# Kernel optimization log

Hardware: AMD Instinct MI355X
Metric: run time of the kernel (lower is better)

Reference implementation:

```python
import jax, jax.numpy as jnp
import numpy as np

B, N, C, H = 32, 197, 768, 12
D = C // H  # head dim = 64


def setup_inputs() -> dict:
    key = jax.random.key(0)
    ks = jax.random.split(key, 5)
    std = 0.02
    x = jax.random.normal(ks[0], (B, N, C), dtype=jnp.float32)
    w_qkv = jax.random.normal(ks[1], (C, 3 * C), dtype=jnp.float32) * std
    w_proj = jax.random.normal(ks[2], (C, C), dtype=jnp.float32) * std
    b_proj = jnp.zeros((C,), dtype=jnp.float32)
    # 1x1 convs over the head axis of the attention map (Conv2d(H,H,1,bias=False))
    w_conv_l = jax.random.normal(ks[3], (H, H), dtype=jnp.float32) * std + jnp.eye(H, dtype=jnp.float32)
    w_conv_w = jax.random.normal(ks[4], (H, H), dtype=jnp.float32) * std + jnp.eye(H, dtype=jnp.float32)
    return {"x": x, "w_qkv": w_qkv, "w_proj": w_proj, "b_proj": b_proj,
            "w_conv_l": w_conv_l, "w_conv_w": w_conv_w}


def reference(x, w_qkv, w_proj, b_proj, w_conv_l, w_conv_w):
    b, n, c = x.shape
    h, d = H, c // H
    scale = d ** (-0.5)
    qkv = (x @ w_qkv).reshape(b, n, 3, h, d).transpose(2, 0, 3, 1, 4)  # [3,B,H,N,D]
    q, k, v = qkv[0], qkv[1], qkv[2]
    # value_map branch (control_output.need_value_map=True)
    value_map = jax.nn.softmax(jnp.einsum('bhnd,bhmd->bhnm', v, v) * scale, axis=-1)
    # scaled QK^T
    attn = jnp.einsum('bhnd,bhmd->bhnm', q * scale, k)  # [B,H,N,N]
    attention_scores = attn  # need_attn_score=True (captured pre-conv)
    # conv_l: 1x1 conv mixing heads
    attn = jnp.einsum('oh,bhnm->bonm', w_conv_l, attn)
    attention_probs = jax.nn.softmax(attn, axis=-1)  # need_attn_prob=True
    # conv_w: 1x1 conv mixing heads on the probabilities
    attn_w = jnp.einsum('oh,bhnm->bonm', w_conv_w, attention_probs)
    out = jnp.einsum('bhnm,bhmd->bhnd', attn_w, v)  # [B,H,N,D]
    out = out.transpose(0, 2, 1, 3).reshape(b, n, c)
    attention_output = out @ w_proj + b_proj
    return attention_output, attention_scores, attention_probs, value_map
```

## Files before the change

kernel.cpp:

```cpp
#include <hip/hip_runtime.h>
#include <cmath>

#define B_ 32
#define N_ 197
#define C_ 768
#define H_ 12
#define D_ 64
#define M_ (B_*N_)
#define MPAD_ 6400
#define K3_ (3*C_)
#define NN_ (N_*N_)
#define BH_ (B_*H_)
#define NP_ 208
#define KP_ 224
#define SCALE 0.125f

typedef __bf16 bf16x8 __attribute__((ext_vector_type(8)));
typedef __bf16 bf16x4 __attribute__((ext_vector_type(4)));
typedef float  f32x4  __attribute__((ext_vector_type(4)));

__device__ __forceinline__ void gl_lds16(const void* g, void* l) {
    __builtin_amdgcn_global_load_lds(
        (const __attribute__((address_space(1))) void*)g,
        (__attribute__((address_space(3))) void*)l,
        16, 0, 0);
}

__global__ __launch_bounds__(256) void cast_x_kernel(const float* __restrict__ X,
        __bf16* __restrict__ Xb) {
    const long long i = ((long long)blockIdx.x * 256 + threadIdx.x) * 4;
    if (i >= (long long)MPAD_ * 768) return;
    bf16x4 o;
    if (i < (long long)M_ * 768) {
        float4 f = *(const float4*)&X[i];
        o.x = (__bf16)f.x; o.y = (__bf16)f.y; o.z = (__bf16)f.z; o.w = (__bf16)f.w;
    } else {
        o.x = o.y = o.z = o.w = (__bf16)0.f;
    }
    *(bf16x4*)&Xb[i] = o;
}

__global__ __launch_bounds__(256) void transpose_cast(const float* __restrict__ W,
        __bf16* __restrict__ Wt, int R, int Ccols) {
    __shared__ float t[32][33];
    const int c0 = blockIdx.x * 32;
    const int r0 = blockIdx.y * 32;
    const int tx = threadIdx.x & 31, ty = threadIdx.x >> 5;
    #pragma unroll
    for (int i = ty; i < 32; i += 8)
        t[i][tx] = W[(size_t)(r0 + i) * Ccols + c0 + tx];
    __syncthreads();
    #pragma unroll
    for (int i = ty; i < 32; i += 8)
        Wt[(size_t)(c0 + i) * R + r0 + tx] = (__bf16)t[tx][i];
}

__global__ __launch_bounds__(256) void mfma_qkv(const __bf16* __restrict__ Xb,
        const __bf16* __restrict__ Wt, __bf16* __restrict__ q,
        __bf16* __restrict__ k, __bf16* __restrict__ v) {
    __shared__ __bf16 As[128*32];
    __shared__ __bf16 Bs[128*32];
    const int tid = threadIdx.x;
    const int wv = tid >> 6, ln = tid & 63;
    const int R0 = blockIdx.x * 128;
    const int C0 = blockIdx.y * 128;
    const int wm = wv >> 1, wn = wv & 1;
    const int arow = ln >> 2, akg = ln & 3;
    f32x4 acc[4][4] = {};
    for (int k0 = 0; k0 < 768; k0 += 32) {
        __syncthreads();
        #pragma unroll
        for (int s = 0; s < 2; s++) {
            const int seg = wv + s*4;
            const int row = seg*16 + arow;
            gl_lds16(Xb + (size_t)(R0 + row)*768 + k0 + akg*8,
                     (char*)As + seg*1024 + ln*16);
            gl_lds16(Wt + (size_t)(C0 + row)*768 + k0 + akg*8,
                     (char*)Bs + seg*1024 + ln*16);
        }
        __syncthreads();
        bf16x8 af[4], bfr[4];
        #pragma unroll
        for (int t = 0; t < 4; t++) {
            af[t]  = *(const bf16x8*)((const char*)As +
                        (wm*64 + t*16 + (ln & 15))*64 + (ln >> 4)*16);
            bfr[t] = *(const bf16x8*)((const char*)Bs +
                        (wn*64 + t*16 + (ln & 15))*64 + (ln >> 4)*16);
        }
        #pragma unroll
        for (int i = 0; i < 4; i++)
            #pragma unroll
            for (int j = 0; j < 4; j++)
                acc[i][j] = __builtin_amdgcn_mfma_f32_16x16x32_bf16(
                                af[i], bfr[j], acc[i][j], 0, 0, 0);
    }
    const int lr = (ln >> 4) * 4;
    const int lc = ln & 15;
    #pragma unroll
    for (int j = 0; j < 4; j++) {
        const int c = C0 + wn*64 + j*16 + lc;
        const int which = c / 768;
        const int rem = c - which*768;
        const int h = rem >> 6, d = rem & 63;
        __bf16* dst = (which == 0) ? q : ((which == 1) ? k : v);
        #pragma unroll
        for (int i = 0; i < 4; i++) {
            #pragma unroll
            for (int rr = 0; rr < 4; rr++) {
                const int r = R0 + wm*64 + i*16 + lr + rr;
                if (r < M_) {
                    const int bb = r / N_, n = r - bb*N_;
                    dst[(((size_t)(bb*H_ + h))*N_ + n)*64 + d] =
                        (__bf16)acc[i][j][rr];
                }
            }
        }
    }
}

__global__ __launch_bounds__(256) void mfma_proj(const __bf16* __restrict__ Ab,
        const __bf16* __restrict__ Wt, const float* __restrict__ bias,
        float* __restrict__ Y) {
    __shared__ __bf16 As[128*32];
    __shared__ __bf16 Bs[128*32];
    const int tid = threadIdx.x;
    const int wv = tid >> 6, ln = tid & 63;
    const int R0 = blockIdx.x * 128;
    const int C0 = blockIdx.y * 128;
    const int wm = wv >> 1, wn = wv & 1;
    const int arow = ln >> 2, akg = ln & 3;
    f32x4 acc[4][4] = {};
    for (int k0 = 0; k0 < 768; k0 += 32) {
        __syncthreads();
        #pragma unroll
        for (int s = 0; s < 2; s++) {
            const int seg = wv + s*4;
            const int row = seg*16 + arow;
            gl_lds16(Ab + (size_t)(R0 + row)*768 + k0 + akg*8,
                     (char*)As + seg*1024 + ln*16);
            gl_lds16(Wt + (size_t)(C0 + row)*768 + k0 + akg*8,
                     (char*)Bs + seg*1024 + ln*16);
        }
        __syncthreads();
        bf16x8 af[4], bfr[4];
        #pragma unroll
        for (int t = 0; t < 4; t++) {
            af[t]  = *(const bf16x8*)((const char*)As +
                        (wm*64 + t*16 + (ln & 15))*64 + (ln >> 4)*16);
            bfr[t] = *(const bf16x8*)((const char*)Bs +
                        (wn*64 + t*16 + (ln & 15))*64 + (ln >> 4)*16);
        }
        #pragma unroll
        for (int i = 0; i < 4; i++)
            #pragma unroll
            for (int j = 0; j < 4; j++)
                acc[i][j] = __builtin_amdgcn_mfma_f32_16x16x32_bf16(
                                af[i], bfr[j], acc[i][j], 0, 0, 0);
    }
    const int lr = (ln >> 4) * 4;
    const int lc = ln & 15;
    #pragma unroll
    for (int j = 0; j < 4; j++) {
        const int c = C0 + wn*64 + j*16 + lc;
        const float bv = bias[c];
        #pragma unroll
        for (int i = 0; i < 4; i++) {
            #pragma unroll
            for (int rr = 0; rr < 4; rr++) {
                const int r = R0 + wm*64 + i*16 + lr + rr;
                if (r < M_) Y[(size_t)r*768 + c] = acc[i][j][rr] + bv;
            }
        }
    }
}

__global__ __launch_bounds__(256) void qkt_vvt(const __bf16* __restrict__ Q,
        const __bf16* __restrict__ Km, const __bf16* __restrict__ V,
        float* __restrict__ S, float* __restrict__ VM) {
    __shared__ __bf16 Al[NP_*64];
    __shared__ __bf16 Bl[NP_*64];
    const int tid = threadIdx.x;
    const int w = tid >> 6, L = tid & 63;
    const int lm = L & 15, lg = L >> 4;
    if (blockIdx.x < BH_) {
        const int bh = blockIdx.x;
        const __bf16* Qb = Q  + (size_t)bh*N_*D_;
        const __bf16* Kb = Km + (size_t)bh*N_*D_;
        for (int i = tid*8; i < NP_*64; i += 2048) {
            const int row = i >> 6;
            bf16x8 z = {};
            *(bf16x8*)&Al[i] = (row < N_) ? *(const bf16x8*)&Qb[i] : z;
            *(bf16x8*)&Bl[i] = (row < N_) ? *(const bf16x8*)&Kb[i] : z;
        }
        __syncthreads();
        for (int rt = w; rt < 13; rt += 4) {
            const bf16x8 a0 = *(const bf16x8*)&Al[(rt*16+lm)*64 + lg*8];
            const bf16x8 a1 = *(const bf16x8*)&Al[(rt*16+lm)*64 + 32 + lg*8];
            const int rbase = rt*16 + lg*4;
            for (int ct = 0; ct < 13; ct++) {
                const bf16x8 b0 = *(const bf16x8*)&Bl[(ct*16+lm)*64 + lg*8];
                const bf16x8 b1 = *(const bf16x8*)&Bl[(ct*16+lm)*64 + 32 + lg*8];
                f32x4 acc = {};
                acc = __builtin_amdgcn_mfma_f32_16x16x32_bf16(a0, b0, acc, 0, 0, 0);
                acc = __builtin_amdgcn_mfma_f32_16x16x32_bf16(a1, b1, acc, 0, 0, 0);
                const int c = ct*16 + lm;
                if (c < N_) {
                    #pragma unroll
                    for (int r = 0; r < 4; r++) {
                        const int row = rbase + r;
                        if (row < N_)
                            S[((size_t)bh*N_ + row)*N_ + c] = acc[r] * SCALE;
                    }
                }
            }
        }
    } else {
        const int bh = blockIdx.x - BH_;
        const __bf16* Vb = V + (size_t)bh*N_*D_;
        for (int i = tid*8; i < NP_*64; i += 2048) {
            const int row = i >> 6;
            bf16x8 z = {};
            *(bf16x8*)&Al[i] = (row < N_) ? *(const bf16x8*)&Vb[i] : z;
        }
        __syncthreads();
        for (int rt = w; rt < 13; rt += 4) {
            const bf16x8 a0 = *(const bf16x8*)&Al[(rt*16+lm)*64 + lg*8];
            const bf16x8 a1 = *(const bf16x8*)&Al[(rt*16+lm)*64 + 32 + lg*8];
            f32x4 acc[13];
            for (int ct = 0; ct < 13; ct++) {
                const bf16x8 b0 = *(const bf16x8*)&Al[(ct*16+lm)*64 + lg*8];
                const bf16x8 b1 = *(const bf16x8*)&Al[(ct*16+lm)*64 + 32 + lg*8];
                f32x4 a = {};
                a = __builtin_amdgcn_mfma_f32_16x16x32_bf16(a0, b0, a, 0, 0, 0);
                a = __builtin_amdgcn_mfma_f32_16x16x32_bf16(a1, b1, a, 0, 0, 0);
                acc[ct] = a;
            }
            float mx[4] = {-1e30f, -1e30f, -1e30f, -1e30f};
            #pragma unroll
            for (int ct = 0; ct < 13; ct++) {
                const bool valid = (ct*16 + lm) < N_;
                #pragma unroll
                for (int r = 0; r < 4; r++) {
                    float val = valid ? acc[ct][r] * SCALE : -1e30f;
                    acc[ct][r] = val;
                    mx[r] = fmaxf(mx[r], val);
                }
            }
            #pragma unroll
            for (int r = 0; r < 4; r++) {
                #pragma unroll
                for (int off = 1; off < 16; off <<= 1)
                    mx[r] = fmaxf(mx[r], __shfl_xor(mx[r], off));
            }
            float sm[4] = {0.f, 0.f, 0.f, 0.f};
            #pragma unroll
            for (int ct = 0; ct < 13; ct++)
                #pragma unroll
                for (int r = 0; r < 4; r++) {
                    const float e = __expf(acc[ct][r] - mx[r]);
                    acc[ct][r] = e;
                    sm[r] += e;
                }
            #pragma unroll
            for (int r = 0; r < 4; r++) {
                #pragma unroll
                for (int off = 1; off < 16; off <<= 1)
                    sm[r] += __shfl_xor(sm[r], off);
                sm[r] = 1.f / sm[r];
            }
            const int rbase = rt*16 + lg*4;
            for (int ct = 0; ct < 13; ct++) {
                const int c = ct*16 + lm;
                if (c < N_) {
                    #pragma unroll
                    for (int r = 0; r < 4; r++) {
                        const int row = rbase + r;
                        if (row < N_)
                            VM[((size_t)bh*N_ + row)*N_ + c] = acc[ct][r] * sm[r];
                    }
                }
            }
        }
    }
}

__global__ __launch_bounds__(256) void convl_convw(const float* __restrict__ SC,
        const float* __restrict__ wl, const float* __restrict__ ww,
        float* __restrict__ PR, __bf16* __restrict__ AW) {
    __shared__ float raw[12*200];
    __shared__ float mixed[12*200];
    __shared__ float wls[144];
    __shared__ float wws[144];
    const int tid = threadIdx.x;
    const int b = blockIdx.x / N_;
    const int n = blockIdx.x - b * N_;
    if (tid < 144) { wls[tid] = wl[tid]; wws[tid] = ww[tid]; }
    for (int i = tid; i < 12*N_; i += 256) {
        int h = i / N_, m = i - h*N_;
        raw[h*200 + m] = SC[(((size_t)(b*12 + h))*N_ + n)*N_ + m];
    }
    __syncthreads();
    for (int i = tid; i < 12*N_; i += 256) {
        int o = i / N_, m = i - o*N_;
        float s = 0.f;
        #pragma unroll
        for (int h = 0; h < 12; h++) s += wls[o*12 + h] * raw[h*200 + m];
        mixed[o*200 + m] = s;
    }
    __syncthreads();
    const int w = tid >> 6, l = tid & 63;
    for (int j = 0; j < 3; j++) {
        const int o = w*3 + j;
        float vv[4];
        float mx = -1e30f;
        #pragma unroll
        for (int c = 0; c < 4; c++) {
            int m = l + 64*c;
            vv[c] = (m < N_) ? mixed[o*200 + m] : -1e30f;
            mx = fmaxf(mx, vv[c]);
        }
        #pragma unroll
        for (int off = 32; off; off >>= 1) mx = fmaxf(mx, __shfl_xor(mx, off));
        float s = 0.f;
        #pragma unroll
        for (int c = 0; c < 4; c++) {
            int m = l + 64*c;
            if (m < N_) { vv[c] = __expf(vv[c] - mx); s += vv[c]; }
        }
        #pragma unroll
        for (int off = 32; off; off >>= 1) s += __shfl_xor(s, off);
        const float inv = 1.f / s;
        float* Prow = PR + (((size_t)(b*12 + o))*N_ + n)*N_;
        #pragma unroll
        for (int c = 0; c < 4; c++) {
            int m = l + 64*c;
            if (m < N_) {
                const float p = vv[c] * inv;
                Prow[m] = p;
                raw[o*200 + m] = p;
            }
        }
    }
    __syncthreads();
    for (int i = tid; i < 12*KP_; i += 256) {
        int o = i / KP_, m = i - o*KP_;
        float s = 0.f;
        if (m < N_) {
            #pragma unroll
            for (int h = 0; h < 12; h++) s += wws[o*12 + h] * raw[h*200 + m];
        }
        AW[((size_t)(b*12 + o)*N_ + n)*KP_ + m] = (__bf16)s;
    }
}

__global__ __launch_bounds__(256) void av_mfma(const __bf16* __restrict__ AW,
        const __bf16* __restrict__ V, __bf16* __restrict__ OP) {
    __shared__ __bf16 Vt[64*KP_];
    const int tid = threadIdx.x, bh = blockIdx.x;
    const int w = tid >> 6, L = tid & 63;
    for (int i = tid*8; i < 64*KP_; i += 2048) {
        bf16x8 z = {};
        *(bf16x8*)&Vt[i] = z;
    }
    __syncthreads();
    const __bf16* Vb = V + (size_t)bh*N_*D_;
    for (int i = tid*8; i < N_*D_; i += 2048) {
        const int row = i >> 6, col = i & 63;
        const bf16x8 vv = *(const bf16x8*)&Vb[i];
        #pragma unroll
        for (int j = 0; j < 8; j++) Vt[(col+j)*KP_ + row] = vv[j];
    }
    __syncthreads();
    const int lm = L & 15, lg = L >> 4;
    const int b = bh / H_, h = bh - b*H_;
    const __bf16* Ab = AW + (size_t)bh*N_*KP_;
    for (int rt = w; rt < 13; rt += 4) {
        int ar = rt*16 + lm;
        if (ar >= N_) ar = 0;
        f32x4 acc[4] = {};
        #pragma unroll
        for (int k0 = 0; k0 < KP_; k0 += 32) {
            const bf16x8 a = *(const bf16x8*)&Ab[(size_t)ar*KP_ + k0 + lg*8];
            #pragma unroll
            for (int ct = 0; ct < 4; ct++) {
                const bf16x8 bf = *(const bf16x8*)&Vt[(ct*16+lm)*KP_ + k0 + lg*8];
                acc[ct] = __builtin_amdgcn_mfma_f32_16x16x32_bf16(
                              a, bf, acc[ct], 0, 0, 0);
            }
        }
        const int rbase = rt*16 + lg*4;
        #pragma unroll
        for (int ct = 0; ct < 4; ct++) {
            const int d = ct*16 + lm;
            #pragma unroll
            for (int r = 0; r < 4; r++) {
                const int row = rbase + r;
                if (row < N_)
                    OP[((size_t)(b*N_ + row))*C_ + h*64 + d] = (__bf16)acc[ct][r];
            }
        }
    }
}

extern "C" void kernel_launch(void* const* d_in, const int* in_sizes, int n_in,
                              void* d_out, int out_size, void* d_ws, size_t ws_size,
                              hipStream_t stream) {
    const float* x      = (const float*)d_in[0];
    const float* w_qkv  = (const float*)d_in[1];
    const float* w_proj = (const float*)d_in[2];
    const float* b_proj = (const float*)d_in[3];
    const float* w_cl   = (const float*)d_in[4];
    const float* w_cw   = (const float*)d_in[5];

    float* out    = (float*)d_out;
    float* scores = out    + (size_t)M_ * C_;
    float* probs  = scores + (size_t)BH_ * NN_;
    float* vmap   = probs  + (size_t)BH_ * NN_;

    char* base = (char*)d_ws;
    const size_t QS = (size_t)BH_ * N_ * D_;
    __bf16* q   = (__bf16*)base;
    __bf16* k   = q + QS;
    __bf16* v   = k + QS;
    __bf16* Xb  = v + QS;
    __bf16* OPb = Xb;
    __bf16* Wqt = Xb + (size_t)MPAD_*768;
    __bf16* Wpt = Wqt + (size_t)K3_*768;
    __bf16* aw  = Wpt + (size_t)768*768;

    cast_x_kernel <<<(MPAD_*768/4 + 255)/256, 256, 0, stream>>>(x, Xb);
    transpose_cast<<<dim3(72, 24),  256, 0, stream>>>(w_qkv,  Wqt, 768, K3_);
    transpose_cast<<<dim3(24, 24),  256, 0, stream>>>(w_proj, Wpt, 768, 768);

    mfma_qkv      <<<dim3(50, 18),  256, 0, stream>>>(Xb, Wqt, q, k, v);
    qkt_vvt       <<<2*BH_,         256, 0, stream>>>(q, k, v, scores, vmap);
    convl_convw   <<<M_,            256, 0, stream>>>(scores, w_cl, w_cw, probs, aw);
    av_mfma       <<<BH_,           256, 0, stream>>>(aw, v, OPb);
    mfma_proj     <<<dim3(50, 6),   256, 0, stream>>>(OPb, Wpt, b_proj, out);
}
```

Baseline: 383.2 us.

## Swizzle LDS layouts and transpose MFMA operands for vectorized score stores

Applies XOR swizzles to the LDS tiles in qkt_vvt and to the transposed V tile in av_mfma, padding the latter to a 256-element stride, to avoid LDS bank conflicts on fragment reads. The QK^T and VV^T MFMAs swap operand order so each lane holds four consecutive columns of one row. This allows 16-byte row stores of scores and value_map instead of scattered scalar stores. The value_map softmax now reduces across lanes with two shuffles instead of four, and each wave keeps its Q fragments in registers while looping over K tiles. Unaligned vector stores and the remapped indexing add correctness risk.

After: 388.9 us. About the same (+1.5%).

```diff
diff --git a/kernel.cpp b/kernel.cpp
--- a/kernel.cpp
+++ b/kernel.cpp
@@ -13,11 +13,13 @@
 #define BH_ (B_*H_)
 #define NP_ 208
 #define KP_ 224
+#define VTS_ 256
 #define SCALE 0.125f
 
 typedef __bf16 bf16x8 __attribute__((ext_vector_type(8)));
 typedef __bf16 bf16x4 __attribute__((ext_vector_type(4)));
 typedef float  f32x4  __attribute__((ext_vector_type(4)));
+typedef float  f32x4u __attribute__((ext_vector_type(4), aligned(4)));
 
 __device__ __forceinline__ void gl_lds16(const void* g, void* l) {
     __builtin_amdgcn_global_load_lds(
@@ -188,28 +190,44 @@
         const __bf16* Kb = Km + (size_t)bh*N_*D_;
         for (int i = tid*8; i < NP_*64; i += 2048) {
             const int row = i >> 6;
+            const int di = (i & ~63) | ((((i >> 3) & 7) ^ (row & 7)) << 3);
             bf16x8 z = {};
-            *(bf16x8*)&Al[i] = (row < N_) ? *(const bf16x8*)&Qb[i] : z;
-            *(bf16x8*)&Bl[i] = (row < N_) ? *(const bf16x8*)&Kb[i] : z;
-        }
-        __syncthreads();
-        for (int rt = w; rt < 13; rt += 4) {
-            const bf16x8 a0 = *(const bf16x8*)&Al[(rt*16+lm)*64 + lg*8];
-            const bf16x8 a1 = *(const bf16x8*)&Al[(rt*16+lm)*64 + 32 + lg*8];
-            const int rbase = rt*16 + lg*4;
-            for (int ct = 0; ct < 13; ct++) {
-                const bf16x8 b0 = *(const bf16x8*)&Bl[(ct*16+lm)*64 + lg*8];
-                const bf16x8 b1 = *(const bf16x8*)&Bl[(ct*16+lm)*64 + 32 + lg*8];
+            *(bf16x8*)&Al[di] = (row < N_) ? *(const bf16x8*)&Qb[i] : z;
+            *(bf16x8*)&Bl[di] = (row < N_) ? *(const bf16x8*)&Kb[i] : z;
+        }
+        __syncthreads();
+        const bool isw0 = (w == 0);
+        int nts[4];
+        nts[0] = w; nts[1] = w + 4; nts[2] = w + 8; nts[3] = isw0 ? 12 : w;
+        bf16x8 qf0[4], qf1[4];
+        #pragma unroll
+        for (int t = 0; t < 4; t++) {
+            const int qr = nts[t]*16 + lm;
+            qf0[t] = *(const bf16x8*)&Al[qr*64 + ((lg ^ (qr & 7)) << 3)];
+            qf1[t] = *(const bf16x8*)&Al[qr*64 + (((4 + lg) ^ (qr & 7)) << 3)];
+        }
+        for (int mt = 0; mt < 13; mt++) {
+            const int kr = mt*16 + lm;
+            const bf16x8 k0 = *(const bf16x8*)&Bl[kr*64 + ((lg ^ (kr & 7)) << 3)];
+            const bf16x8 k1 = *(const bf16x8*)&Bl[kr*64 + (((4 + lg) ^ (kr & 7)) << 3)];
+            const int m0 = mt*16 + lg*4;
+            #pragma unroll
+            for (int t = 0; t < 4; t++) {
                 f32x4 acc = {};
-                acc = __builtin_amdgcn_mfma_f32_16x16x32_bf16(a0, b0, acc, 0, 0, 0);
-                acc = __builtin_amdgcn_mfma_f32_16x16x32_bf16(a1, b1, acc, 0, 0, 0);
-                const int c = ct*16 + lm;
-                if (c < N_) {
-                    #pragma unroll
-                    for (int r = 0; r < 4; r++) {
-                        const int row = rbase + r;
-                        if (row < N_)
-                            S[((size_t)bh*N_ + row)*N_ + c] = acc[r] * SCALE;
+                acc = __builtin_amdgcn_mfma_f32_16x16x32_bf16(k0, qf0[t], acc, 0, 0, 0);
+                acc = __builtin_amdgcn_mfma_f32_16x16x32_bf16(k1, qf1[t], acc, 0, 0, 0);
+                const int n = nts[t]*16 + lm;
+                if ((t < 3 || isw0) && n < N_) {
+                    float* Srow = S + ((size_t)bh*N_ + n)*N_;
+                    if (m0 + 3 < N_) {
+                        f32x4 st;
+                        #pragma unroll
+                        for (int r = 0; r < 4; r++) st[r] = acc[r] * SCALE;
+                        *(f32x4u*)&Srow[m0] = st;
+                    } else {
+                        #pragma unroll
+                        for (int r = 0; r < 4; r++)
+                            if (m0 + r < N_) Srow[m0 + r] = acc[r] * SCALE;
                     }
                 }
             }
@@ -219,65 +237,65 @@
         const __bf16* Vb = V + (size_t)bh*N_*D_;
         for (int i = tid*8; i < NP_*64; i += 2048) {
             const int row = i >> 6;
+            const int di = (i & ~63) | ((((i >> 3) & 7) ^ (row & 7)) << 3);
             bf16x8 z = {};
-            *(bf16x8*)&Al[i] = (row < N_) ? *(const bf16x8*)&Vb[i] : z;
-        }
-        __syncthreads();
-        for (int rt = w; rt < 13; rt += 4) {
-            const bf16x8 a0 = *(const bf16x8*)&Al[(rt*16+lm)*64 + lg*8];
-            const bf16x8 a1 = *(const bf16x8*)&Al[(rt*16+lm)*64 + 32 + lg*8];
+            *(bf16x8*)&Al[di] = (row < N_) ? *(const bf16x8*)&Vb[i] : z;
+        }
+        __syncthreads();
+        for (int nt = w; nt < 13; nt += 4) {
+            const int qr = nt*16 + lm;
+            const bf16x8 q0 = *(const bf16x8*)&Al[qr*64 + ((lg ^ (qr & 7)) << 3)];
+            const bf16x8 q1 = *(const bf16x8*)&Al[qr*64 + (((4 + lg) ^ (qr & 7)) << 3)];
             f32x4 acc[13];
-            for (int ct = 0; ct < 13; ct++) {
-                const bf16x8 b0 = *(const bf16x8*)&Al[(ct*16+lm)*64 + lg*8];
-                const bf16x8 b1 = *(const bf16x8*)&Al[(ct*16+lm)*64 + 32 + lg*8];
+            for (int mt = 0; mt < 13; mt++) {
+                const int kr = mt*16 + lm;
+                const bf16x8 a0 = *(const bf16x8*)&Al[kr*64 + ((lg ^ (kr & 7)) << 3)];
+                const bf16x8 a1 = *(const bf16x8*)&Al[kr*64 + (((4 + lg) ^ (kr & 7)) << 3)];
                 f32x4 a = {};
-                a = __builtin_amdgcn_mfma_f32_16x16x32_bf16(a0, b0, a, 0, 0, 0);
-                a = __builtin_amdgcn_mfma_f32_16x16x32_bf16(a1, b1, a, 0, 0, 0);
-                acc[ct] = a;
-            }
-            float mx[4] = {-1e30f, -1e30f, -1e30f, -1e30f};
-            #pragma unroll
-            for (int ct = 0; ct < 13; ct++) {
-                const bool valid = (ct*16 + lm) < N_;
+                a = __builtin_amdgcn_mfma_f32_16x16x32_bf16(a0, q0, a, 0, 0, 0);
+                a = __builtin_amdgcn_mfma_f32_16x16x32_bf16(a1, q1, a, 0, 0, 0);
+                acc[mt] = a;
+            }
+            #pragma unroll
+            for (int mt = 0; mt < 13; mt++)
+                #pragma unroll
+                for (int r = 0; r < 4; r++) acc[mt][r] *= SCALE;
+            #pragma unroll
+            for (int r = 0; r < 4; r++)
+                if (192 + lg*4 + r >= N_) acc[12][r] = -1e30f;
+            float mx = -1e30f;
+            #pragma unroll
+            for (int mt = 0; mt < 13; mt++)
+                #pragma unroll
+                for (int r = 0; r < 4; r++) mx = fmaxf(mx, acc[mt][r]);
+            mx = fmaxf(mx, __shfl_xor(mx, 16));
+            mx = fmaxf(mx, __shfl_xor(mx, 32));
+            float sm = 0.f;
+            #pragma unroll
+            for (int mt = 0; mt < 13; mt++)
                 #pragma unroll
                 for (int r = 0; r < 4; r++) {
-                    float val = valid ? acc[ct][r] * SCALE : -1e30f;
-                    acc[ct][r] = val;
-                    mx[r] = fmaxf(mx[r], val);
+                    const float e = __expf(acc[mt][r] - mx);
+                    acc[mt][r] = e;
+                    sm += e;
                 }
-            }
-            #pragma unroll
-            for (int r = 0; r < 4; r++) {
+            sm += __shfl_xor(sm, 16);
+            sm += __shfl_xor(sm, 32);
+            const float inv = 1.f / sm;
+            const int n = qr;
+            if (n < N_) {
+                float* Vrow = VM + ((size_t)bh*N_ + n)*N_;
                 #pragma unroll
-                for (int off = 1; off < 16; off <<= 1)
-                    mx[r] = fmaxf(mx[r], __shfl_xor(mx[r], off));
-            }
-            float sm[4] = {0.f, 0.f, 0.f, 0.f};
-            #pragma unroll
-            for (int ct = 0; ct < 13; ct++)
+                for (int mt = 0; mt < 12; mt++) {
+                    f32x4 st;
+                    #pragma unroll
+                    for (int r = 0; r < 4; r++) st[r] = acc[mt][r] * inv;
+                    *(f32x4u*)&Vrow[mt*16 + lg*4] = st;
+                }
                 #pragma unroll
                 for (int r = 0; r < 4; r++) {
-                    const float e = __expf(acc[ct][r] - mx[r]);
-                    acc[ct][r] = e;
-                    sm[r] += e;
-                }
-            #pragma unroll
-            for (int r = 0; r < 4; r++) {
-                #pragma unroll
-                for (int off = 1; off < 16; off <<= 1)
-                    sm[r] += __shfl_xor(sm[r], off);
-                sm[r] = 1.f / sm[r];
-            }
-            const int rbase = rt*16 + lg*4;
-            for (int ct = 0; ct < 13; ct++) {
-                const int c = ct*16 + lm;
-                if (c < N_) {
-                    #pragma unroll
-                    for (int r = 0; r < 4; r++) {
-                        const int row = rbase + r;
-                        if (row < N_)
-                            VM[((size_t)bh*N_ + row)*N_ + c] = acc[ct][r] * sm[r];
-                    }
+                    const int m = 192 + lg*4 + r;
+                    if (m < N_) Vrow[m] = acc[12][r] * inv;
                 }
             }
         }
@@ -355,10 +373,10 @@
 
 __global__ __launch_bounds__(256) void av_mfma(const __bf16* __restrict__ AW,
         const __bf16* __restrict__ V, __bf16* __restrict__ OP) {
-    __shared__ __bf16 Vt[64*KP_];
+    __shared__ __bf16 Vt[64*VTS_];
     const int tid = threadIdx.x, bh = blockIdx.x;
     const int w = tid >> 6, L = tid & 63;
-    for (int i = tid*8; i < 64*KP_; i += 2048) {
+    for (int i = tid*8; i < 64*VTS_; i += 2048) {
         bf16x8 z = {};
         *(bf16x8*)&Vt[i] = z;
     }
@@ -368,7 +386,10 @@
         const int row = i >> 6, col = i & 63;
         const bf16x8 vv = *(const bf16x8*)&Vb[i];
         #pragma unroll
-        for (int j = 0; j < 8; j++) Vt[(col+j)*KP_ + row] = vv[j];
+        for (int j = 0; j < 8; j++) {
+            const int d = col + j;
+            Vt[d*VTS_ + ((((row >> 3) ^ (d & 7)) << 3) | (row & 7))] = vv[j];
+        }
     }
     __syncthreads();
     const int lm = L & 15, lg = L >> 4;
@@ -383,7 +404,9 @@
             const bf16x8 a = *(const bf16x8*)&Ab[(size_t)ar*KP_ + k0 + lg*8];
             #pragma unroll
             for (int ct = 0; ct < 4; ct++) {
-                const bf16x8 bf = *(const bf16x8*)&Vt[(ct*16+lm)*KP_ + k0 + lg*8];
+                const int dr = ct*16 + lm;
+                const bf16x8 bf = *(const bf16x8*)
+                    &Vt[dr*VTS_ + ((((k0 >> 3) + lg) ^ (lm & 7)) << 3)];
                 acc[ct] = __builtin_amdgcn_mfma_f32_16x16x32_bf16(
                               a, bf, acc[ct], 0, 0, 0);
             }
```
